# Kernel optimization log

Measured on AMD Instinct MI355X. Metric: run time of the kernel, lower is better.

Reference implementation:

```python
import jax, jax.numpy as jnp
import numpy as np

N, E, G = 50000, 800000, 64   # nodes, edges, graphs
F, H, O = 6, 256, 2           # in_dim, hidden_dim, out_dim
NE, K, L = 8, 2, 4            # n_experts, top_k, n_layers


def setup_inputs() -> dict:
    key = jax.random.key(0)
    ks = jax.random.split(key, 12)
    s = 0.05
    return {
        "x": jax.random.normal(ks[0], (N, F), jnp.float32),
        "edge_index": jax.random.randint(ks[1], (2, E), 0, N),
        "batch": jnp.sort(jax.random.randint(ks[2], (N,), 0, G)),
        "enc_W": jax.random.normal(ks[3], (F, H), jnp.float32) * s,
        "enc_b": jnp.zeros((H,), jnp.float32),
        "rtr_W1": jax.random.normal(ks[4], (H + 2, H), jnp.float32) * s,
        "rtr_b1": jnp.zeros((H,), jnp.float32),
        "rtr_W2": jax.random.normal(ks[5], (H, NE), jnp.float32) * s,
        "rtr_b2": jnp.zeros((NE,), jnp.float32),
        "hid_Wr": jax.random.normal(ks[6], (L - 1, NE, H, H), jnp.float32) * s,
        "hid_Wn": jax.random.normal(ks[7], (L - 1, NE, H, H), jnp.float32) * s,
        "hid_b": jnp.zeros((L - 1, NE, H), jnp.float32),
        "out_Wr": jax.random.normal(ks[8], (NE, H, O), jnp.float32) * s,
        "out_Wn": jax.random.normal(ks[9], (NE, H, O), jnp.float32) * s,
        "out_b": jnp.zeros((NE, O), jnp.float32),
    }


def reference(x, edge_index, batch, enc_W, enc_b, rtr_W1, rtr_b1, rtr_W2, rtr_b2,
              hid_Wr, hid_Wn, hid_b, out_Wr, out_Wn, out_b):
    src, dst = edge_index[0], edge_index[1]

    # SharedBusEncoder: Linear + ReLU
    h = jax.nn.relu(x @ enc_W + enc_b)  # [N, H]

    # graph_size_features: per-graph node/edge counts, log-scaled, per node
    ones_n = jnp.ones((N,), h.dtype)
    nodes_per_g = jax.ops.segment_sum(ones_n, batch, num_segments=G)
    edges_per_g = jax.ops.segment_sum(jnp.ones((E,), h.dtype), batch[src], num_segments=G)
    size_feat = jnp.stack([jnp.log(nodes_per_g + 1.0)[batch],
                           jnp.log(edges_per_g + 1.0)[batch]], axis=-1)  # [N, 2]

    # BaseRouter: 2-layer MLP -> logits [N, NE]
    r = jax.nn.relu(jnp.concatenate([h, size_feat], axis=-1) @ rtr_W1 + rtr_b1)
    logits = r @ rtr_W2 + rtr_b2

    # sparse_routing (eval mode): softmax over top-k logits, scattered to dense mask
    vals, idx = jax.lax.top_k(logits, K)  # [N, K]
    w = jax.nn.softmax(vals, axis=-1)
    sparse = jnp.zeros((N, NE), h.dtype).at[jnp.arange(N)[:, None], idx].set(w)

    # Dense all-expert GraphConv stacks, mask-sum combine
    def graph_conv(he, Wr, Wn, b):
        agg = jax.ops.segment_sum(he[src], dst, num_segments=N)  # sum-aggregate neighbors
        return he @ Wr + agg @ Wn + b

    out = jnp.zeros((N, O), h.dtype)
    for e in range(NE):
        he = h
        for l in range(L - 1):
            he = jax.nn.relu(graph_conv(he, hid_Wr[l, e], hid_Wn[l, e], hid_b[l, e]))
        ye = graph_conv(he, out_Wr[e], out_Wn[e], out_b[e])  # [N, O]
        out = out + ye * sparse[:, e:e + 1]
    return out
```

## Files before the change

### kernel.cpp

```cpp
#include <hip/hip_runtime.h>
#include <cstdint>

#define NN 50000
#define EE 800000
#define GG 64

typedef unsigned short u16;
typedef __attribute__((ext_vector_type(8))) short bf16x8;
typedef __attribute__((ext_vector_type(4))) float f32x4;

__device__ __forceinline__ float bf2f(u16 v) { return __uint_as_float(((unsigned)v) << 16); }
__device__ __forceinline__ u16 f2bf(float f) {
  unsigned u = __float_as_uint(f);
  return (u16)((u + 0x7fffu + ((u >> 16) & 1u)) >> 16);
}

__device__ __forceinline__ void gload_lds16(const void* g, void* l) {
  __builtin_amdgcn_global_load_lds(
      (const __attribute__((address_space(1))) void*)g,
      (__attribute__((address_space(3))) void*)l,
      16, 0, 0);
}

__global__ void k_sentinel(float* out) { out[threadIdx.x] = 1e12f; }

__global__ __launch_bounds__(256) void k_encoder(
    const float* __restrict__ x, const float* __restrict__ W,
    const float* __restrict__ b, u16* __restrict__ hb) {
  int idx = blockIdx.x * 256 + threadIdx.x;
  if (idx >= NN * 256) return;
  int row = idx >> 8, j = idx & 255;
  float s = b[j];
#pragma unroll
  for (int k = 0; k < 6; ++k) s += x[row * 6 + k] * W[k * 256 + j];
  hb[idx] = f2bf(fmaxf(s, 0.f));
}

__global__ __launch_bounds__(256) void k_outdeg(const int* __restrict__ src,
                                                int* __restrict__ outdeg) {
  int i = blockIdx.x * 256 + threadIdx.x;
  if (i < EE) atomicAdd(&outdeg[src[i]], 1);
}

__global__ __launch_bounds__(256) void k_graph_feats(const int* __restrict__ batch,
                                                     const int* __restrict__ outdeg,
                                                     float* __restrict__ gf) {
  __shared__ int red[256];
  int g = blockIdx.x, tid = threadIdx.x;
  auto lb = [&](int v) {
    int lo = 0, hi = NN;
    while (lo < hi) { int m = (lo + hi) >> 1; if (batch[m] < v) lo = m + 1; else hi = m; }
    return lo;
  };
  int bs = lb(g), be = lb(g + 1);
  int s = 0;
  for (int i = bs + tid; i < be; i += 256) s += outdeg[i];
  red[tid] = s;
  __syncthreads();
  for (int off = 128; off > 0; off >>= 1) {
    if (tid < off) red[tid] += red[tid + off];
    __syncthreads();
  }
  if (tid == 0) {
    gf[g * 2] = logf((float)(be - bs) + 1.f);
    gf[g * 2 + 1] = logf((float)red[0] + 1.f);
  }
}

__global__ __launch_bounds__(256) void k_router(
    const float* __restrict__ x, const float* __restrict__ encW, const float* __restrict__ encb,
    const int* __restrict__ batch, const float* __restrict__ gf,
    const float* __restrict__ W1, const float* __restrict__ b1,
    const float* __restrict__ W2, const float* __restrict__ b2,
    float* __restrict__ sparse) {
  __shared__ __align__(16) float hs_t[258][8];
  __shared__ __align__(16) float rs_t[256][8];
  __shared__ float xv[8][6];
  __shared__ float sf[8][2];
  __shared__ float lg[8][8];
  int tid = threadIdx.x;
  int nb = blockIdx.x * 8;
  if (tid < 48) {
    int r = tid / 6, k = tid % 6;
    int node = nb + r;
    xv[r][k] = (node < NN) ? x[node * 6 + k] : 0.f;
  }
  if (tid >= 48 && tid < 56) {
    int r = tid - 48;
    int node = nb + r;
    int g = (node < NN) ? batch[node] : 0;
    sf[r][0] = gf[g * 2];
    sf[r][1] = gf[g * 2 + 1];
  }
  __syncthreads();
  {
    float wcol[6];
#pragma unroll
    for (int k = 0; k < 6; ++k) wcol[k] = encW[k * 256 + tid];
    float bb = encb[tid];
#pragma unroll
    for (int r = 0; r < 8; ++r) {
      float s = bb;
#pragma unroll
      for (int k = 0; k < 6; ++k) s += xv[r][k] * wcol[k];
      hs_t[tid][r] = fmaxf(s, 0.f);
    }
  }
  if (tid < 16) {
    int r = tid >> 1, c = tid & 1;
    hs_t[256 + c][r] = sf[r][c];
  }
  __syncthreads();
  float acc[8];
  {
    float bb = b1[tid];
#pragma unroll
    for (int r = 0; r < 8; ++r) acc[r] = bb;
  }
  for (int k = 0; k < 258; ++k) {
    float w = W1[k * 256 + tid];
    float4 ha = *(const float4*)&hs_t[k][0];
    float4 hb4 = *(const float4*)&hs_t[k][4];
    acc[0] += ha.x * w; acc[1] += ha.y * w; acc[2] += ha.z * w; acc[3] += ha.w * w;
    acc[4] += hb4.x * w; acc[5] += hb4.y * w; acc[6] += hb4.z * w; acc[7] += hb4.w * w;
  }
#pragma unroll
  for (int r = 0; r < 8; ++r) rs_t[tid][r] = fmaxf(acc[r], 0.f);
  __syncthreads();
  if (tid < 64) {
    int r = tid >> 3, e = tid & 7;
    float s = b2[e];
    for (int k = 0; k < 256; ++k) s += rs_t[k][r] * W2[k * 8 + e];
    lg[r][e] = s;
  }
  __syncthreads();
  if (tid < 8) {
    int node = nb + tid;
    if (node < NN) {
      float v1 = lg[tid][0];
      int j1 = 0;
#pragma unroll
      for (int j = 1; j < 8; ++j) {
        float v = lg[tid][j];
        if (v > v1) { v1 = v; j1 = j; }
      }
      float v2 = -1e30f;
      int j2 = 0;
#pragma unroll
      for (int j = 0; j < 8; ++j) {
        if (j == j1) continue;
        float v = lg[tid][j];
        if (v > v2) { v2 = v; j2 = j; }
      }
      float ex = expf(v2 - v1);
      float wa = 1.f / (1.f + ex), wb = ex / (1.f + ex);
      float* sp = sparse + node * 8;
#pragma unroll
      for (int j = 0; j < 8; ++j) sp[j] = 0.f;
      sp[j1] = wa;
      sp[j2] = wb;
    }
  }
}

__global__ __launch_bounds__(256) void k_deg(const int* __restrict__ dst, int* __restrict__ deg) {
  int i = blockIdx.x * 256 + threadIdx.x;
  if (i < EE) atomicAdd(&deg[dst[i]], 1);
}

__global__ __launch_bounds__(1024) void k_scan(const int* __restrict__ deg,
                                               int* __restrict__ rowptr) {
  __shared__ int tmp[1024];
  __shared__ int carry;
  if (threadIdx.x == 0) { carry = 0; rowptr[0] = 0; }
  __syncthreads();
  for (int base = 0; base < NN; base += 1024) {
    int i = base + threadIdx.x;
    int v = (i < NN) ? deg[i] : 0;
    tmp[threadIdx.x] = v;
    __syncthreads();
    for (int off = 1; off < 1024; off <<= 1) {
      int t = (threadIdx.x >= off) ? tmp[threadIdx.x - off] : 0;
      __syncthreads();
      tmp[threadIdx.x] += t;
      __syncthreads();
    }
    if (i < NN) rowptr[i + 1] = carry + tmp[threadIdx.x];
    int last = tmp[1023];
    __syncthreads();
    if (threadIdx.x == 0) carry += last;
    __syncthreads();
  }
}

__global__ __launch_bounds__(256) void k_fill(const int* __restrict__ ei,
                                              const int* __restrict__ rowptr,
                                              int* __restrict__ cursor, int* __restrict__ csrc) {
  int i = blockIdx.x * 256 + threadIdx.x;
  if (i < EE) {
    int s = ei[i], d = ei[EE + i];
    int pos = atomicAdd(&cursor[d], 1);
    csrc[rowptr[d] + pos] = s;
  }
}

__global__ __launch_bounds__(256) void k_spmm256(
    const int* __restrict__ rowptr, const int* __restrict__ csrc,
    const u16* __restrict__ Xb, size_t xs, u16* __restrict__ Yb, size_t ys) {
  const u16* X = Xb + (size_t)blockIdx.y * xs;
  u16* Y = Yb + (size_t)blockIdx.y * ys;
  int wave = threadIdx.x >> 6, lane = threadIdx.x & 63;
  int d = blockIdx.x * 4 + wave;
  if (d >= NN) return;
  int s0 = rowptr[d], s1 = rowptr[d + 1];
  int c4 = lane * 4;
  float a0 = 0.f, a1 = 0.f, a2 = 0.f, a3 = 0.f;
  int i = s0;
  for (; i + 2 <= s1; i += 2) {
    int sa = csrc[i], sb = csrc[i + 1];
    ushort4 va = *(const ushort4*)(X + sa * 256 + c4);
    ushort4 vb = *(const ushort4*)(X + sb * 256 + c4);
    a0 += bf2f(va.x) + bf2f(vb.x);
    a1 += bf2f(va.y) + bf2f(vb.y);
    a2 += bf2f(va.z) + bf2f(vb.z);
    a3 += bf2f(va.w) + bf2f(vb.w);
  }
  if (i < s1) {
    int sa = csrc[i];
    ushort4 va = *(const ushort4*)(X + sa * 256 + c4);
    a0 += bf2f(va.x);
    a1 += bf2f(va.y);
    a2 += bf2f(va.z);
    a3 += bf2f(va.w);
  }
  ushort4 o;
  o.x = f2bf(a0); o.y = f2bf(a1); o.z = f2bf(a2); o.w = f2bf(a3);
  *(ushort4*)(Y + d * 256 + c4) = o;
}

__global__ __launch_bounds__(256) void k_transpose(const float* __restrict__ W,
                                                   u16* __restrict__ Wt, int nmat) {
  int idx = blockIdx.x * 256 + threadIdx.x;
  if (idx >= nmat * 65536) return;
  int m = idx >> 16, rem = idx & 65535;
  int k = rem >> 8, j = rem & 255;
  Wt[(m << 16) + (j << 8) + k] = f2bf(W[idx]);
}

__global__ __launch_bounds__(512) void k_gemm(
    const u16* __restrict__ X1b, size_t x1s, const u16* __restrict__ X2b, size_t x2s,
    const u16* __restrict__ W1tb, const u16* __restrict__ W2tb, size_t wst,
    const float* __restrict__ biasb, size_t bst,
    u16* __restrict__ Yb, size_t yst, int relu) {
  __shared__ __align__(16) u16 Alds[2][128 * 32];
  __shared__ __align__(16) u16 Blds[2][256 * 32];
  int g = blockIdx.y;
  const u16* X1 = X1b + (size_t)g * x1s;
  const u16* X2 = X2b + (size_t)g * x2s;
  const u16* W1t = W1tb + (size_t)g * wst;
  const u16* W2t = W2tb + (size_t)g * wst;
  const float* bias = biasb + (size_t)g * bst;
  u16* Y = Yb + (size_t)g * yst;
  int tid = threadIdx.x;
  int wave = tid >> 6, lane = tid & 63;
  int l15 = lane & 15, l4 = lane >> 4;
  int m0 = blockIdx.x * 128;
  int wr = wave >> 2, wc = wave & 3;
  const f32x4 fz = {0.f, 0.f, 0.f, 0.f};
  f32x4 acc[4][4];
#pragma unroll
  for (int a = 0; a < 4; ++a)
#pragma unroll
    for (int b = 0; b < 4; ++b) acc[a][b] = fz;

  auto stage = [&](int t) {
    const u16* xs = (t < 8) ? X1 : X2;
    const u16* wsrc = (t < 8) ? W1t : W2t;
    int kb = (t & 7) * 32;
    int half = t & 1;
    {
      int flat = wave * 1024 + lane * 16;
      int row = flat >> 6, colb = flat & 63;
      int scol = colb ^ (((row >> 1) & 3) << 4);
      int gr = m0 + row;
      if (gr > NN - 1) gr = NN - 1;
      gload_lds16(xs + gr * 256 + kb + (scol >> 1), (char*)Alds[half] + flat);
    }
#pragma unroll
    for (int q = 0; q < 2; ++q) {
      int flat = q * 8192 + wave * 1024 + lane * 16;
      int row = flat >> 6, colb = flat & 63;
      int scol = colb ^ (((row >> 1) & 3) << 4);
      gload_lds16(wsrc + row * 256 + kb + (scol >> 1), (char*)Blds[half] + flat);
    }
  };

  stage(0);
  for (int kt = 0; kt < 16; ++kt) {
    if (kt < 15) {
      stage(kt + 1);
      asm volatile("s_waitcnt vmcnt(3)" ::: "memory");
    } else {
      asm volatile("s_waitcnt vmcnt(0)" ::: "memory");
    }
    __builtin_amdgcn_sched_barrier(0);
    __builtin_amdgcn_s_barrier();
    __builtin_amdgcn_sched_barrier(0);
    const char* Ab = (const char*)Alds[kt & 1];
    const char* Bb = (const char*)Blds[kt & 1];
    bf16x8 af[4], bfv[4];
#pragma unroll
    for (int mi = 0; mi < 4; ++mi) {
      int r = wr * 64 + mi * 16 + l15;
      af[mi] = *(const bf16x8*)(Ab + r * 64 + ((l4 * 16) ^ (((r >> 1) & 3) << 4)));
    }
#pragma unroll
    for (int nj = 0; nj < 4; ++nj) {
      int c = wc * 64 + nj * 16 + l15;
      bfv[nj] = *(const bf16x8*)(Bb + c * 64 + ((l4 * 16) ^ (((c >> 1) & 3) << 4)));
    }
#pragma unroll
    for (int mi = 0; mi < 4; ++mi)
#pragma unroll
      for (int nj = 0; nj < 4; ++nj)
        acc[mi][nj] =
            __builtin_amdgcn_mfma_f32_16x16x32_bf16(af[mi], bfv[nj], acc[mi][nj], 0, 0, 0);
    __builtin_amdgcn_sched_barrier(0);
    __builtin_amdgcn_s_barrier();
  }
#pragma unroll
  for (int mi = 0; mi < 4; ++mi) {
    int rbase = m0 + wr * 64 + mi * 16 + l4 * 4;
#pragma unroll
    for (int nj = 0; nj < 4; ++nj) {
      int col = wc * 64 + nj * 16 + l15;
      float bv = bias[col];
#pragma unroll
      for (int r2 = 0; r2 < 4; ++r2) {
        int row = rbase + r2;
        if (row < NN) {
          float v = acc[mi][nj][r2] + bv;
          if (relu) v = fmaxf(v, 0.f);
          Y[row * 256 + col] = f2bf(v);
        }
      }
    }
  }
}

__global__ __launch_bounds__(256) void k_outproj(
    const u16* __restrict__ heb, size_t hes, const float* __restrict__ oWr,
    const float* __restrict__ oWn, int e0, float* __restrict__ Y4self,
    float* __restrict__ Y4nb) {
  __shared__ float Ws[256 * 4];
  int eabs = e0 + blockIdx.y;
  const u16* he = heb + (size_t)blockIdx.y * hes;
  const float* Wr = oWr + eabs * 512;
  const float* Wn = oWn + eabs * 512;
  int tid = threadIdx.x;
  Ws[tid * 4 + 0] = Wr[tid * 2];
  Ws[tid * 4 + 1] = Wr[tid * 2 + 1];
  Ws[tid * 4 + 2] = Wn[tid * 2];
  Ws[tid * 4 + 3] = Wn[tid * 2 + 1];
  __syncthreads();
  int wave = tid >> 6, lane = tid & 63;
  int node = blockIdx.x * 4 + wave;
  if (node >= NN) return;
  const u16* hrow = he + node * 256;
  int k0 = lane * 4;
  ushort4 hv4 = *(const ushort4*)(hrow + k0);
  float hv[4] = {bf2f(hv4.x), bf2f(hv4.y), bf2f(hv4.z), bf2f(hv4.w)};
  float a0 = 0.f, a1 = 0.f, a2 = 0.f, a3 = 0.f;
#pragma unroll
  for (int t = 0; t < 4; ++t) {
    float hvv = hv[t];
    const float* w = Ws + (k0 + t) * 4;
    a0 += hvv * w[0];
    a1 += hvv * w[1];
    a2 += hvv * w[2];
    a3 += hvv * w[3];
  }
#pragma unroll
  for (int off = 32; off > 0; off >>= 1) {
    a0 += __shfl_down(a0, off);
    a1 += __shfl_down(a1, off);
    a2 += __shfl_down(a2, off);
    a3 += __shfl_down(a3, off);
  }
  if (lane == 0) {
    Y4self[node * 16 + eabs * 2] = a0;
    Y4self[node * 16 + eabs * 2 + 1] = a1;
    Y4nb[node * 16 + eabs * 2] = a2;
    Y4nb[node * 16 + eabs * 2 + 1] = a3;
  }
}

__global__ __launch_bounds__(256) void k_combine(
    const int* __restrict__ rowptr, const int* __restrict__ csrc,
    const float* __restrict__ Y4self, const float* __restrict__ Y4nb,
    const float* __restrict__ sparse, const float* __restrict__ ob,
    float* __restrict__ out) {
  int t = blockIdx.x * 256 + threadIdx.x;
  int d = t >> 3, e = t & 7;
  if (d >= NN) return;
  float s0 = Y4self[d * 16 + e * 2], s1 = Y4self[d * 16 + e * 2 + 1];
  float n0 = 0.f, n1 = 0.f;
  for (int i = rowptr[d]; i < rowptr[d + 1]; ++i) {
    int s = csrc[i];
    float2 v = *(const float2*)(Y4nb + s * 16 + e * 2);
    n0 += v.x;
    n1 += v.y;
  }
  float w = sparse[d * 8 + e];
  float t0 = w * (s0 + n0 + ob[e * 2]);
  float t1 = w * (s1 + n1 + ob[e * 2 + 1]);
  t0 += __shfl_xor(t0, 1); t1 += __shfl_xor(t1, 1);
  t0 += __shfl_xor(t0, 2); t1 += __shfl_xor(t1, 2);
  t0 += __shfl_xor(t0, 4); t1 += __shfl_xor(t1, 4);
  if (e == 0) {
    out[d * 2] = t0;
    out[d * 2 + 1] = t1;
  }
}

extern "C" void kernel_launch(void* const* d_in, const int* in_sizes, int n_in,
                              void* d_out, int out_size, void* d_ws, size_t ws_size,
                              hipStream_t stream) {
  const float* x = (const float*)d_in[0];
  const int* ei = (const int*)d_in[1];
  const int* batch = (const int*)d_in[2];
  const float* enc_W = (const float*)d_in[3];
  const float* enc_b = (const float*)d_in[4];
  const float* rW1 = (const float*)d_in[5];
  const float* rb1 = (const float*)d_in[6];
  const float* rW2 = (const float*)d_in[7];
  const float* rb2 = (const float*)d_in[8];
  const float* hid_Wr = (const float*)d_in[9];
  const float* hid_Wn = (const float*)d_in[10];
  const float* hid_b = (const float*)d_in[11];
  const float* out_Wr = (const float*)d_in[12];
  const float* out_Wn = (const float*)d_in[13];
  const float* out_b = (const float*)d_in[14];
  float* out = (float*)d_out;

  char* ws = (char*)d_ws;
  size_t off = 0;
  auto alloc = [&](size_t bytes) -> void* {
    void* p = ws + off;
    off = (off + bytes + 511) & ~(size_t)511;
    return p;
  };
  const size_t HBYTES = (size_t)NN * 256 * 2;
  u16* hb = (u16*)alloc(HBYTES);
  u16* agg0 = (u16*)alloc(HBYTES);
  u16* WrT = (u16*)alloc((size_t)24 * 65536 * 2);
  u16* WnT = (u16*)alloc((size_t)24 * 65536 * 2);
  int* deg = (int*)alloc((size_t)NN * 4);
  int* rowptr = (int*)alloc((size_t)(NN + 1) * 4);
  int* cursor = (int*)alloc((size_t)NN * 4);
  int* outdeg = (int*)alloc((size_t)NN * 4);
  int* csrc = (int*)alloc((size_t)EE * 4);
  float* gf = (float*)alloc(GG * 2 * 4);
  float* sparse = (float*)alloc((size_t)NN * 8 * 4);
  float* Y4self = (float*)alloc((size_t)NN * 16 * 4);
  float* Y4nb = (float*)alloc((size_t)NN * 16 * 4);

  size_t rem = (ws_size > off) ? ws_size - off : 0;
  size_t per = 2 * HBYTES + 2048;
  int grp = (rem >= 4 * per) ? 4 : (rem >= 2 * per) ? 2 : (rem >= per) ? 1 : 0;
  if (grp == 0) {
    k_sentinel<<<1, 2, 0, stream>>>(out);
    return;
  }
  u16* heb = (u16*)alloc((size_t)grp * HBYTES);
  u16* aggb = (u16*)alloc((size_t)grp * HBYTES);

  hipMemsetAsync(deg, 0, (size_t)NN * 4, stream);
  hipMemsetAsync(cursor, 0, (size_t)NN * 4, stream);
  hipMemsetAsync(outdeg, 0, (size_t)NN * 4, stream);

  k_encoder<<<(NN * 256 + 255) / 256, 256, 0, stream>>>(x, enc_W, enc_b, hb);
  k_transpose<<<(24 * 65536 + 255) / 256, 256, 0, stream>>>(hid_Wr, WrT, 24);
  k_transpose<<<(24 * 65536 + 255) / 256, 256, 0, stream>>>(hid_Wn, WnT, 24);
  k_outdeg<<<(EE + 255) / 256, 256, 0, stream>>>(ei, outdeg);
  k_graph_feats<<<GG, 256, 0, stream>>>(batch, outdeg, gf);
  k_router<<<NN / 8, 256, 0, stream>>>(x, enc_W, enc_b, batch, gf, rW1, rb1, rW2, rb2, sparse);
  k_deg<<<(EE + 255) / 256, 256, 0, stream>>>(ei + EE, deg);
  k_scan<<<1, 1024, 0, stream>>>(deg, rowptr);
  k_fill<<<(EE + 255) / 256, 256, 0, stream>>>(ei, rowptr, cursor, csrc);

  const int GX = (NN + 127) / 128;
  const int SX = (NN + 3) / 4;
  const size_t HS = (size_t)NN * 256;

  k_spmm256<<<dim3(SX, 1), 256, 0, stream>>>(rowptr, csrc, hb, 0, agg0, 0);
  for (int e0 = 0; e0 < 8; e0 += grp) {
    k_gemm<<<dim3(GX, grp), 512, 0, stream>>>(
        hb, 0, agg0, 0, WrT + e0 * 65536, WnT + e0 * 65536, 65536,
        hid_b + e0 * 256, 256, heb, HS, 1);
    for (int l = 1; l < 3; ++l) {
      k_spmm256<<<dim3(SX, grp), 256, 0, stream>>>(rowptr, csrc, heb, HS, aggb, HS);
      k_gemm<<<dim3(GX, grp), 512, 0, stream>>>(
          heb, HS, aggb, HS, WrT + (l * 8 + e0) * 65536, WnT + (l * 8 + e0) * 65536, 65536,
          hid_b + (l * 8 + e0) * 256, 256, heb, HS, 1);
    }
    k_outproj<<<dim3(SX, grp), 256, 0, stream>>>(heb, HS, out_Wr, out_Wn, e0, Y4self, Y4nb);
  }
  k_combine<<<(NN * 8 + 255) / 256, 256, 0, stream>>>(rowptr, csrc, Y4self, Y4nb, sparse,
                                                      out_b, out);
}
```

Before: 2.519 ms.

## Fuse output projection into last hidden GEMM epilogue and merge setup kernels

The final hidden-layer GEMM epilogue now applies bias and ReLU, projects onto the expert's 2-column output weights with a shuffle and LDS reduction, and writes Y4self/Y4nb directly. This removes the bf16 write of the last hidden activation and the separate k_outproj pass that re-read it. Setup is also consolidated: the two degree histograms share one kernel, the two weight transposes share one kernel, and three memsets become one. The router's second matmul is split across all threads with partial sums, and its first loop is unrolled. In exchange the GEMM kernel carries extra parameters and a larger epilogue, which may raise register pressure.

```diff
diff --git a/kernel.cpp b/kernel.cpp
--- a/kernel.cpp
+++ b/kernel.cpp
@@ -36,10 +36,14 @@
   hb[idx] = f2bf(fmaxf(s, 0.f));
 }
 
-__global__ __launch_bounds__(256) void k_outdeg(const int* __restrict__ src,
-                                                int* __restrict__ outdeg) {
+__global__ __launch_bounds__(256) void k_hist(const int* __restrict__ ei,
+                                              int* __restrict__ deg,
+                                              int* __restrict__ outdeg) {
   int i = blockIdx.x * 256 + threadIdx.x;
-  if (i < EE) atomicAdd(&outdeg[src[i]], 1);
+  if (i < EE) {
+    atomicAdd(&outdeg[ei[i]], 1);
+    atomicAdd(&deg[ei[EE + i]], 1);
+  }
 }
 
 __global__ __launch_bounds__(256) void k_graph_feats(const int* __restrict__ batch,
@@ -75,6 +79,7 @@
     float* __restrict__ sparse) {
   __shared__ __align__(16) float hs_t[258][8];
   __shared__ __align__(16) float rs_t[256][8];
+  __shared__ float part2[4][64];
   __shared__ float xv[8][6];
   __shared__ float sf[8][2];
   __shared__ float lg[8][8];
@@ -117,21 +122,38 @@
 #pragma unroll
     for (int r = 0; r < 8; ++r) acc[r] = bb;
   }
-  for (int k = 0; k < 258; ++k) {
+  int k = 0;
+#pragma unroll 4
+  for (; k < 256; ++k) {
     float w = W1[k * 256 + tid];
     float4 ha = *(const float4*)&hs_t[k][0];
     float4 hb4 = *(const float4*)&hs_t[k][4];
     acc[0] += ha.x * w; acc[1] += ha.y * w; acc[2] += ha.z * w; acc[3] += ha.w * w;
     acc[4] += hb4.x * w; acc[5] += hb4.y * w; acc[6] += hb4.z * w; acc[7] += hb4.w * w;
   }
+  for (; k < 258; ++k) {
+    float w = W1[k * 256 + tid];
+    float4 ha = *(const float4*)&hs_t[k][0];
+    float4 hb4 = *(const float4*)&hs_t[k][4];
+    acc[0] += ha.x * w; acc[1] += ha.y * w; acc[2] += ha.z * w; acc[3] += ha.w * w;
+    acc[4] += hb4.x * w; acc[5] += hb4.y * w; acc[6] += hb4.z * w; acc[7] += hb4.w * w;
+  }
 #pragma unroll
   for (int r = 0; r < 8; ++r) rs_t[tid][r] = fmaxf(acc[r], 0.f);
+  __syncthreads();
+  {
+    int pr = tid & 63, pt = tid >> 6;
+    int r = pr >> 3, e = pr & 7;
+    float s = 0.f;
+    int kk0 = pt * 64;
+#pragma unroll 4
+    for (int kk = kk0; kk < kk0 + 64; ++kk) s += rs_t[kk][r] * W2[kk * 8 + e];
+    part2[pt][pr] = s;
+  }
   __syncthreads();
   if (tid < 64) {
     int r = tid >> 3, e = tid & 7;
-    float s = b2[e];
-    for (int k = 0; k < 256; ++k) s += rs_t[k][r] * W2[k * 8 + e];
-    lg[r][e] = s;
+    lg[r][e] = b2[e] + part2[0][tid] + part2[1][tid] + part2[2][tid] + part2[3][tid];
   }
   __syncthreads();
   if (tid < 8) {
@@ -161,11 +183,6 @@
       sp[j2] = wb;
     }
   }
-}
-
-__global__ __launch_bounds__(256) void k_deg(const int* __restrict__ dst, int* __restrict__ deg) {
-  int i = blockIdx.x * 256 + threadIdx.x;
-  if (i < EE) atomicAdd(&deg[dst[i]], 1);
 }
 
 __global__ __launch_bounds__(1024) void k_scan(const int* __restrict__ deg,
@@ -238,22 +255,27 @@
   *(ushort4*)(Y + d * 256 + c4) = o;
 }
 
-__global__ __launch_bounds__(256) void k_transpose(const float* __restrict__ W,
-                                                   u16* __restrict__ Wt, int nmat) {
+__global__ __launch_bounds__(256) void k_transpose2(const float* __restrict__ Wr,
+                                                    const float* __restrict__ Wn,
+                                                    u16* __restrict__ WrT,
+                                                    u16* __restrict__ WnT) {
   int idx = blockIdx.x * 256 + threadIdx.x;
-  if (idx >= nmat * 65536) return;
+  if (idx >= 24 * 65536) return;
   int m = idx >> 16, rem = idx & 65535;
   int k = rem >> 8, j = rem & 255;
-  Wt[(m << 16) + (j << 8) + k] = f2bf(W[idx]);
+  int o = (m << 16) + (j << 8) + k;
+  WrT[o] = f2bf(Wr[idx]);
+  WnT[o] = f2bf(Wn[idx]);
 }
 
 __global__ __launch_bounds__(512) void k_gemm(
     const u16* __restrict__ X1b, size_t x1s, const u16* __restrict__ X2b, size_t x2s,
     const u16* __restrict__ W1tb, const u16* __restrict__ W2tb, size_t wst,
     const float* __restrict__ biasb, size_t bst,
-    u16* __restrict__ Yb, size_t yst, int relu) {
-  __shared__ __align__(16) u16 Alds[2][128 * 32];
-  __shared__ __align__(16) u16 Blds[2][256 * 32];
+    u16* __restrict__ Yb, size_t yst, int relu,
+    const float* __restrict__ oWr, const float* __restrict__ oWn, int e0_base,
+    float* __restrict__ Y4self, float* __restrict__ Y4nb, int do_out) {
+  __shared__ __align__(16) char smem[49152];
   int g = blockIdx.y;
   const u16* X1 = X1b + (size_t)g * x1s;
   const u16* X2 = X2b + (size_t)g * x2s;
@@ -284,14 +306,14 @@
       int scol = colb ^ (((row >> 1) & 3) << 4);
       int gr = m0 + row;
       if (gr > NN - 1) gr = NN - 1;
-      gload_lds16(xs + gr * 256 + kb + (scol >> 1), (char*)Alds[half] + flat);
+      gload_lds16(xs + gr * 256 + kb + (scol >> 1), smem + half * 8192 + flat);
     }
 #pragma unroll
     for (int q = 0; q < 2; ++q) {
       int flat = q * 8192 + wave * 1024 + lane * 16;
       int row = flat >> 6, colb = flat & 63;
       int scol = colb ^ (((row >> 1) & 3) << 4);
-      gload_lds16(wsrc + row * 256 + kb + (scol >> 1), (char*)Blds[half] + flat);
+      gload_lds16(wsrc + row * 256 + kb + (scol >> 1), smem + 16384 + half * 16384 + flat);
     }
   };
 
@@ -306,8 +328,8 @@
     __builtin_amdgcn_sched_barrier(0);
     __builtin_amdgcn_s_barrier();
     __builtin_amdgcn_sched_barrier(0);
-    const char* Ab = (const char*)Alds[kt & 1];
-    const char* Bb = (const char*)Blds[kt & 1];
+    const char* Ab = smem + (kt & 1) * 8192;
+    const char* Bb = smem + 16384 + (kt & 1) * 16384;
     bf16x8 af[4], bfv[4];
 #pragma unroll
     for (int mi = 0; mi < 4; ++mi) {
@@ -328,70 +350,78 @@
     __builtin_amdgcn_sched_barrier(0);
     __builtin_amdgcn_s_barrier();
   }
-#pragma unroll
-  for (int mi = 0; mi < 4; ++mi) {
-    int rbase = m0 + wr * 64 + mi * 16 + l4 * 4;
+
+  if (!do_out) {
+#pragma unroll
+    for (int mi = 0; mi < 4; ++mi) {
+      int rbase = m0 + wr * 64 + mi * 16 + l4 * 4;
+#pragma unroll
+      for (int nj = 0; nj < 4; ++nj) {
+        int col = wc * 64 + nj * 16 + l15;
+        float bv = bias[col];
+#pragma unroll
+        for (int r2 = 0; r2 < 4; ++r2) {
+          int row = rbase + r2;
+          if (row < NN) {
+            float v = acc[mi][nj][r2] + bv;
+            if (relu) v = fmaxf(v, 0.f);
+            Y[row * 256 + col] = f2bf(v);
+          }
+        }
+      }
+    }
+  } else {
+    int eabs = e0_base + g;
+    const float2* wr2p = (const float2*)(oWr + (size_t)eabs * 512);
+    const float2* wn2p = (const float2*)(oWn + (size_t)eabs * 512);
+    float bv[4]; float2 wa[4], wb[4];
 #pragma unroll
     for (int nj = 0; nj < 4; ++nj) {
       int col = wc * 64 + nj * 16 + l15;
-      float bv = bias[col];
+      bv[nj] = bias[col];
+      wa[nj] = wr2p[col];
+      wb[nj] = wn2p[col];
+    }
+    float* y4red = (float*)smem;
+#pragma unroll
+    for (int mi = 0; mi < 4; ++mi) {
 #pragma unroll
       for (int r2 = 0; r2 < 4; ++r2) {
-        int row = rbase + r2;
-        if (row < NN) {
-          float v = acc[mi][nj][r2] + bv;
-          if (relu) v = fmaxf(v, 0.f);
-          Y[row * 256 + col] = f2bf(v);
+        float p0 = 0.f, p1 = 0.f, p2 = 0.f, p3 = 0.f;
+#pragma unroll
+        for (int nj = 0; nj < 4; ++nj) {
+          float v = fmaxf(acc[mi][nj][r2] + bv[nj], 0.f);
+          p0 += v * wa[nj].x; p1 += v * wa[nj].y;
+          p2 += v * wb[nj].x; p3 += v * wb[nj].y;
+        }
+#pragma unroll
+        for (int off2 = 1; off2 < 16; off2 <<= 1) {
+          p0 += __shfl_xor(p0, off2); p1 += __shfl_xor(p1, off2);
+          p2 += __shfl_xor(p2, off2); p3 += __shfl_xor(p3, off2);
+        }
+        if (l15 == 0) {
+          int lr = wr * 64 + mi * 16 + l4 * 4 + r2;
+          float* q = y4red + (lr * 4 + wc) * 4;
+          q[0] = p0; q[1] = p1; q[2] = p2; q[3] = p3;
         }
       }
     }
-  }
-}
-
-__global__ __launch_bounds__(256) void k_outproj(
-    const u16* __restrict__ heb, size_t hes, const float* __restrict__ oWr,
-    const float* __restrict__ oWn, int e0, float* __restrict__ Y4self,
-    float* __restrict__ Y4nb) {
-  __shared__ float Ws[256 * 4];
-  int eabs = e0 + blockIdx.y;
-  const u16* he = heb + (size_t)blockIdx.y * hes;
-  const float* Wr = oWr + eabs * 512;
-  const float* Wn = oWn + eabs * 512;
-  int tid = threadIdx.x;
-  Ws[tid * 4 + 0] = Wr[tid * 2];
-  Ws[tid * 4 + 1] = Wr[tid * 2 + 1];
-  Ws[tid * 4 + 2] = Wn[tid * 2];
-  Ws[tid * 4 + 3] = Wn[tid * 2 + 1];
-  __syncthreads();
-  int wave = tid >> 6, lane = tid & 63;
-  int node = blockIdx.x * 4 + wave;
-  if (node >= NN) return;
-  const u16* hrow = he + node * 256;
-  int k0 = lane * 4;
-  ushort4 hv4 = *(const ushort4*)(hrow + k0);
-  float hv[4] = {bf2f(hv4.x), bf2f(hv4.y), bf2f(hv4.z), bf2f(hv4.w)};
-  float a0 = 0.f, a1 = 0.f, a2 = 0.f, a3 = 0.f;
-#pragma unroll
-  for (int t = 0; t < 4; ++t) {
-    float hvv = hv[t];
-    const float* w = Ws + (k0 + t) * 4;
-    a0 += hvv * w[0];
-    a1 += hvv * w[1];
-    a2 += hvv * w[2];
-    a3 += hvv * w[3];
-  }
-#pragma unroll
-  for (int off = 32; off > 0; off >>= 1) {
-    a0 += __shfl_down(a0, off);
-    a1 += __shfl_down(a1, off);
-    a2 += __shfl_down(a2, off);
-    a3 += __shfl_down(a3, off);
-  }
-  if (lane == 0) {
-    Y4self[node * 16 + eabs * 2] = a0;
-    Y4self[node * 16 + eabs * 2 + 1] = a1;
-    Y4nb[node * 16 + eabs * 2] = a2;
-    Y4nb[node * 16 + eabs * 2 + 1] = a3;
+    __syncthreads();
+    if (tid < 128) {
+      int row = m0 + tid;
+      if (row < NN) {
+        float s0 = 0.f, s1 = 0.f, n0 = 0.f, n1 = 0.f;
+#pragma unroll
+        for (int w2 = 0; w2 < 4; ++w2) {
+          const float* q = y4red + (tid * 4 + w2) * 4;
+          s0 += q[0]; s1 += q[1]; n0 += q[2]; n1 += q[3];
+        }
+        Y4self[row * 16 + eabs * 2] = s0;
+        Y4self[row * 16 + eabs * 2 + 1] = s1;
+        Y4nb[row * 16 + eabs * 2] = n0;
+        Y4nb[row * 16 + eabs * 2 + 1] = n1;
+      }
+    }
   }
 }
 
@@ -456,9 +486,10 @@
   u16* WrT = (u16*)alloc((size_t)24 * 65536 * 2);
   u16* WnT = (u16*)alloc((size_t)24 * 65536 * 2);
   int* deg = (int*)alloc((size_t)NN * 4);
-  int* rowptr = (int*)alloc((size_t)(NN + 1) * 4);
   int* cursor = (int*)alloc((size_t)NN * 4);
   int* outdeg = (int*)alloc((size_t)NN * 4);
+  size_t zero_bytes = (size_t)((char*)(outdeg + NN) - (char*)deg);
+  int* rowptr = (int*)alloc((size_t)(NN + 1) * 4);
   int* csrc = (int*)alloc((size_t)EE * 4);
   float* gf = (float*)alloc(GG * 2 * 4);
   float* sparse = (float*)alloc((size_t)NN * 8 * 4);
@@ -475,19 +506,15 @@
   u16* heb = (u16*)alloc((size_t)grp * HBYTES);
   u16* aggb = (u16*)alloc((size_t)grp * HBYTES);
 
-  hipMemsetAsync(deg, 0, (size_t)NN * 4, stream);
-  hipMemsetAsync(cursor, 0, (size_t)NN * 4, stream);
-  hipMemsetAsync(outdeg, 0, (size_t)NN * 4, stream);
+  hipMemsetAsync(deg, 0, zero_bytes, stream);
 
   k_encoder<<<(NN * 256 + 255) / 256, 256, 0, stream>>>(x, enc_W, enc_b, hb);
-  k_transpose<<<(24 * 65536 + 255) / 256, 256, 0, stream>>>(hid_Wr, WrT, 24);
-  k_transpose<<<(24 * 65536 + 255) / 256, 256, 0, stream>>>(hid_Wn, WnT, 24);
-  k_outdeg<<<(EE + 255) / 256, 256, 0, stream>>>(ei, outdeg);
+  k_transpose2<<<(24 * 65536 + 255) / 256, 256, 0, stream>>>(hid_Wr, hid_Wn, WrT, WnT);
+  k_hist<<<(EE + 255) / 256, 256, 0, stream>>>(ei, deg, outdeg);
   k_graph_feats<<<GG, 256, 0, stream>>>(batch, outdeg, gf);
-  k_router<<<NN / 8, 256, 0, stream>>>(x, enc_W, enc_b, batch, gf, rW1, rb1, rW2, rb2, sparse);
-  k_deg<<<(EE + 255) / 256, 256, 0, stream>>>(ei + EE, deg);
   k_scan<<<1, 1024, 0, stream>>>(deg, rowptr);
   k_fill<<<(EE + 255) / 256, 256, 0, stream>>>(ei, rowptr, cursor, csrc);
+  k_router<<<NN / 8, 256, 0, stream>>>(x, enc_W, enc_b, batch, gf, rW1, rb1, rW2, rb2, sparse);
 
   const int GX = (NN + 127) / 128;
   const int SX = (NN + 3) / 4;
@@ -497,14 +524,15 @@
   for (int e0 = 0; e0 < 8; e0 += grp) {
     k_gemm<<<dim3(GX, grp), 512, 0, stream>>>(
         hb, 0, agg0, 0, WrT + e0 * 65536, WnT + e0 * 65536, 65536,
-        hid_b + e0 * 256, 256, heb, HS, 1);
-    for (int l = 1; l < 3; ++l) {
-      k_spmm256<<<dim3(SX, grp), 256, 0, stream>>>(rowptr, csrc, heb, HS, aggb, HS);
-      k_gemm<<<dim3(GX, grp), 512, 0, stream>>>(
-          heb, HS, aggb, HS, WrT + (l * 8 + e0) * 65536, WnT + (l * 8 + e0) * 65536, 65536,
-          hid_b + (l * 8 + e0) * 256, 256, heb, HS, 1);
-    }
-    k_outproj<<<dim3(SX, grp), 256, 0, stream>>>(heb, HS, out_Wr, out_Wn, e0, Y4self, Y4nb);
+        hid_b + e0 * 256, 256, heb, HS, 1, nullptr, nullptr, 0, nullptr, nullptr, 0);
+    k_spmm256<<<dim3(SX, grp), 256, 0, stream>>>(rowptr, csrc, heb, HS, aggb, HS);
+    k_gemm<<<dim3(GX, grp), 512, 0, stream>>>(
+        heb, HS, aggb, HS, WrT + (8 + e0) * 65536, WnT + (8 + e0) * 65536, 65536,
+        hid_b + (8 + e0) * 256, 256, heb, HS, 1, nullptr, nullptr, 0, nullptr, nullptr, 0);
+    k_spmm256<<<dim3(SX, grp), 256, 0, stream>>>(rowptr, csrc, heb, HS, aggb, HS);
+    k_gemm<<<dim3(GX, grp), 512, 0, stream>>>(
+        heb, HS, aggb, HS, WrT + (16 + e0) * 65536, WnT + (16 + e0) * 65536, 65536,
+        hid_b + (16 + e0) * 256, 256, heb, HS, 1, out_Wr, out_Wn, e0, Y4self, Y4nb, 1);
   }
   k_combine<<<(NN * 8 + 255) / 256, 256, 0, stream>>>(rowptr, csrc, Y4self, Y4nb, sparse,
                                                       out_b, out);
```

New measurement: 2.313 ms. 8.2% less time.
